# Optimization experiments

Hardware: AMD Instinct MI355X
Metric: run time of the kernel (lower is better)

The kernel has to match this reference:

```python
import jax, jax.numpy as jnp
import numpy as np

B, S, D, H = 2, 2048, 1024, 16
DK = D // H


def setup_inputs() -> dict:
    key = jax.random.key(0)
    ks = jax.random.split(key, 12)
    sc = 1.0 / np.sqrt(D)
    return {
        "q": jax.random.normal(ks[0], (B, S, D), jnp.float32),
        "k": jax.random.normal(ks[1], (B, S, D), jnp.float32),
        "v": jax.random.normal(ks[2], (B, S, D), jnp.float32),
        "mask": jax.random.randint(ks[3], (B, S), 0, 2, jnp.int32),
        "Wq": jax.random.normal(ks[4], (D, D), jnp.float32) * sc,
        "bq": jnp.zeros((D,), jnp.float32),
        "Wk": jax.random.normal(ks[5], (D, D), jnp.float32) * sc,
        "bk": jnp.zeros((D,), jnp.float32),
        "Wv": jax.random.normal(ks[6], (D, D), jnp.float32) * sc,
        "bv": jnp.zeros((D,), jnp.float32),
        "Wo": jax.random.normal(ks[7], (D, D), jnp.float32) * sc,
        "bo": jnp.zeros((D,), jnp.float32),
    }


def reference(q, k, v, mask, Wq, bq, Wk, bk, Wv, bv, Wo, bo):
    # Projections (flax nn.Dense: x @ W + b)
    query = q @ Wq + bq          # [B,S,D]
    key_ = k @ Wk + bk
    value = v @ Wv + bv
    # split heads -> [B,H,S,DK]
    def split(x):
        return x.reshape(B, S, H, DK).transpose(0, 2, 1, 3)
    qh, kh, vh = split(query), split(key_), split(value)
    scores = jnp.einsum('bhqd,bhkd->bhqk', qh, kh) / jnp.sqrt(jnp.float32(DK))
    # Faithful to source: mask=(mask==0); where(mask==0, -1e10, scores)
    # i.e. positions where ORIGINAL mask != 0 are set to -1e10.
    m = (mask == 0)[:, None, None, :]          # [B,1,1,S] bool
    scores = jnp.where(~m, jnp.float32(-1e10), scores)
    attn = jax.nn.softmax(scores, axis=-1)     # dropout deterministic (eval)
    x = jnp.einsum('bhqk,bhkd->bhqd', attn, vh)
    x = x.transpose(0, 2, 1, 3).reshape(B, S, D)
    return x @ Wo + bo
```

## Files before the change

### kernel.cpp

```cpp
#include <hip/hip_runtime.h>
#include <hip/hip_bf16.h>

typedef unsigned short u16;
typedef unsigned int u32;
typedef __attribute__((ext_vector_type(8))) __bf16 bf16x8;
typedef __attribute__((ext_vector_type(4))) float f32x4;
typedef __attribute__((ext_vector_type(16))) float f32x16;

constexpr int Bz = 2, Sq = 2048, Dm = 1024, Hn = 16, DK = 64;

__device__ __forceinline__ u16 f2bf(float f) {
    u32 u = __builtin_bit_cast(u32, f);
    return (u16)((u + 0x7FFFu + ((u >> 16) & 1u)) >> 16);
}

__device__ __forceinline__ u32 pack_bf16(float a, float b) {
#if __has_builtin(__builtin_amdgcn_cvt_pk_bf16_f32)
    return __builtin_bit_cast(u32, __builtin_amdgcn_cvt_pk_bf16_f32(a, b));
#else
    return (u32)f2bf(a) | ((u32)f2bf(b) << 16);
#endif
}

__device__ __forceinline__ bf16x8 lds_frag(const u16* p) {
    return __builtin_bit_cast(bf16x8, *(const uint4*)p);
}
__device__ __forceinline__ bf16x8 gfrag(const u16* p) {
    return __builtin_bit_cast(bf16x8, *(const uint4*)p);
}
__device__ __forceinline__ int swz(int r) { return (r ^ (r >> 3)) & 7; }

__device__ __forceinline__ void gll16(const u16* g, u16* l) {
    __builtin_amdgcn_global_load_lds(
        (const __attribute__((address_space(1))) void*)g,
        (__attribute__((address_space(3))) void*)l, 16, 0, 0);
}

__global__ __launch_bounds__(256) void mha_prep(
    const float* __restrict__ q, const float* __restrict__ k,
    const float* __restrict__ v,
    const float* __restrict__ w0, const float* __restrict__ w1,
    const float* __restrict__ w2, const float* __restrict__ w3,
    const int* __restrict__ mask,
    u16* __restrict__ qkv_dst, u16* __restrict__ wt_dst,
    float* __restrict__ biasg, int* __restrict__ compg, int* __restrict__ nkg)
{
    __shared__ float tl[64 * 65];
    __shared__ int sc[256];
    const int z = blockIdx.z, tid = threadIdx.x;
    if (z < 3) {
        const float* s = (z == 0) ? q : (z == 1) ? k : v;
        u16* d = qkv_dst + (size_t)z * 4 * 1024 * 1024;
        size_t i = ((size_t)blockIdx.x * 256 + tid) * 8;
        float4 a = *(const float4*)(s + i);
        float4 b = *(const float4*)(s + i + 4);
        *(uint4*)(d + i) = make_uint4(pack_bf16(a.x, a.y), pack_bf16(a.z, a.w),
                                      pack_bf16(b.x, b.y), pack_bf16(b.z, b.w));
        return;
    }
    const int bx = blockIdx.x;
    if (bx >= 1026) return;
    if (bx >= 1024) {
        const int b = bx - 1024;
        const int* mp = mask + b * Sq;
        int4 m0_ = ((const int4*)mp)[tid * 2];
        int4 m1_ = ((const int4*)mp)[tid * 2 + 1];
        int a[8];
        a[0] = (m0_.x == 0); a[1] = (m0_.y == 0); a[2] = (m0_.z == 0); a[3] = (m0_.w == 0);
        a[4] = (m1_.x == 0); a[5] = (m1_.y == 0); a[6] = (m1_.z == 0); a[7] = (m1_.w == 0);
        int cnt = 0;
#pragma unroll
        for (int j = 0; j < 8; j++) cnt += a[j];
        sc[tid] = cnt;
        __syncthreads();
        for (int off = 1; off < 256; off <<= 1) {
            int u = (tid >= off) ? sc[tid - off] : 0;
            int vv = sc[tid];
            __syncthreads();
            sc[tid] = vv + u;
            __syncthreads();
        }
        const int incl = sc[tid];
        const int nk = sc[255];
        int pa = incl - cnt;
        int pi = nk + tid * 8 - pa;
        int* cp = compg + b * Sq;
        float* bbp = biasg + b * Sq;
#pragma unroll
        for (int j = 0; j < 8; j++) {
            int pos = a[j] ? pa++ : pi++;
            cp[tid * 8 + j] = pos;
            bbp[pos] = a[j] ? 0.f : -1.44269504e10f;
        }
        if (tid == 0) nkg[b] = nk;
        return;
    }
    const int zi = bx >> 8, t = bx & 255, tr = t >> 4, tc = t & 15;
    const float* src = (zi == 0) ? w0 : (zi == 1) ? w1 : (zi == 2) ? w2 : w3;
    u16* d = wt_dst + (size_t)zi * Dm * Dm;
    {
        int r = tid >> 2, cq = (tid & 3) * 16;
        const float* sp = src + (size_t)(tr * 64 + r) * Dm + tc * 64 + cq;
#pragma unroll
        for (int j = 0; j < 4; j++) {
            float4 vv = *(const float4*)(sp + j * 4);
            tl[r * 65 + cq + j * 4 + 0] = vv.x;
            tl[r * 65 + cq + j * 4 + 1] = vv.y;
            tl[r * 65 + cq + j * 4 + 2] = vv.z;
            tl[r * 65 + cq + j * 4 + 3] = vv.w;
        }
    }
    __syncthreads();
    {
        int rr = tid >> 2, cc = (tid & 3) * 16;
        u16* dp = d + (size_t)(tc * 64 + rr) * Dm + tr * 64 + cc;
        u32 px[8];
#pragma unroll
        for (int j = 0; j < 8; j++)
            px[j] = pack_bf16(tl[(cc + 2 * j) * 65 + rr], tl[(cc + 2 * j + 1) * 65 + rr]);
        *(uint4*)dp       = make_uint4(px[0], px[1], px[2], px[3]);
        *(uint4*)(dp + 8) = make_uint4(px[4], px[5], px[6], px[7]);
    }
}

__device__ __forceinline__ void gemm_core_128128(
    const u16* __restrict__ Ab, const u16* __restrict__ Bb,
    u16* As, u16* Bs, f32x4 (&acc)[4][4])
{
    const int tid = threadIdx.x, lane = tid & 63;
    const int wm = (tid >> 7) & 1, wn = (tid >> 6) & 1;
    const int frow = lane & 15, quad = lane >> 4;

#pragma unroll
    for (int mi = 0; mi < 4; mi++)
#pragma unroll
        for (int ni = 0; ni < 4; ni++) acc[mi][ni] = (f32x4){0.f, 0.f, 0.f, 0.f};

    for (int k0 = 0; k0 < 1024; k0 += 64) {
#pragma unroll
        for (int i = 0; i < 4; i++) {
            int id = tid + i * 256, r = id >> 3, c = id & 7;
            gll16(Ab + (size_t)r * 1024 + k0 + (c ^ swz(r)) * 8, As + (size_t)id * 8);
        }
#pragma unroll
        for (int i = 0; i < 4; i++) {
            int id = tid + i * 256, r = id >> 3, c = id & 7;
            gll16(Bb + (size_t)r * 1024 + k0 + (c ^ swz(r)) * 8, Bs + (size_t)id * 8);
        }
        __syncthreads();
#pragma unroll
        for (int ks = 0; ks < 2; ks++) {
            bf16x8 af[4], bfr[4];
#pragma unroll
            for (int mi = 0; mi < 4; mi++) {
                int r = wm * 64 + mi * 16 + frow;
                af[mi] = lds_frag(As + r * 64 + ((ks * 4 + quad) ^ swz(r)) * 8);
            }
#pragma unroll
            for (int ni = 0; ni < 4; ni++) {
                int r = wn * 64 + ni * 16 + frow;
                bfr[ni] = lds_frag(Bs + r * 64 + ((ks * 4 + quad) ^ swz(r)) * 8);
            }
#pragma unroll
            for (int mi = 0; mi < 4; mi++)
#pragma unroll
                for (int ni = 0; ni < 4; ni++)
                    acc[mi][ni] = __builtin_amdgcn_mfma_f32_16x16x32_bf16(
                        af[mi], bfr[ni], acc[mi][ni], 0, 0, 0);
        }
        __syncthreads();
    }
}

__device__ __forceinline__ void gemm_core_12864(
    const u16* __restrict__ Ab, const u16* __restrict__ Bb,
    u16* As, u16* Bs, f32x4 (&acc)[4][2])
{
    const int tid = threadIdx.x, lane = tid & 63;
    const int wm = (tid >> 7) & 1, wn = (tid >> 6) & 1;
    const int frow = lane & 15, quad = lane >> 4;

#pragma unroll
    for (int mi = 0; mi < 4; mi++)
#pragma unroll
        for (int ni = 0; ni < 2; ni++) acc[mi][ni] = (f32x4){0.f, 0.f, 0.f, 0.f};

    for (int k0 = 0; k0 < 1024; k0 += 64) {
#pragma unroll
        for (int i = 0; i < 4; i++) {
            int id = tid + i * 256, r = id >> 3, c = id & 7;
            gll16(Ab + (size_t)r * 1024 + k0 + (c ^ swz(r)) * 8, As + (size_t)id * 8);
        }
#pragma unroll
        for (int i = 0; i < 2; i++) {
            int id = tid + i * 256, r = id >> 3, c = id & 7;
            gll16(Bb + (size_t)r * 1024 + k0 + (c ^ swz(r)) * 8, Bs + (size_t)id * 8);
        }
        __syncthreads();
#pragma unroll
        for (int ks = 0; ks < 2; ks++) {
            bf16x8 af[4], bfr[2];
#pragma unroll
            for (int mi = 0; mi < 4; mi++) {
                int r = wm * 64 + mi * 16 + frow;
                af[mi] = lds_frag(As + r * 64 + ((ks * 4 + quad) ^ swz(r)) * 8);
            }
#pragma unroll
            for (int ni = 0; ni < 2; ni++) {
                int r = wn * 32 + ni * 16 + frow;
                bfr[ni] = lds_frag(Bs + r * 64 + ((ks * 4 + quad) ^ swz(r)) * 8);
            }
#pragma unroll
            for (int mi = 0; mi < 4; mi++)
#pragma unroll
                for (int ni = 0; ni < 2; ni++)
                    acc[mi][ni] = __builtin_amdgcn_mfma_f32_16x16x32_bf16(
                        af[mi], bfr[ni], acc[mi][ni], 0, 0, 0);
        }
        __syncthreads();
    }
}

__global__ __launch_bounds__(256, 3) void mha_proj_qkv(
    const u16* __restrict__ Qb, const u16* __restrict__ Kb, const u16* __restrict__ Vb,
    const u16* __restrict__ Wqt, const u16* __restrict__ Wkt, const u16* __restrict__ Wvt,
    const float* __restrict__ bq, const float* __restrict__ bk, const float* __restrict__ bv,
    const int* __restrict__ comp,
    u16* __restrict__ Qh, u16* __restrict__ Kh, u16* __restrict__ Vt)
{
    __shared__ __align__(16) u16 As[128 * 64];
    __shared__ __align__(16) u16 Bs[128 * 64];
    const int z = blockIdx.z, bx = blockIdx.x;
    const u16* Ab; const u16* Bb; const float* bias;
    int m0, n0;
    if (z < 2) {
        m0 = (bx & 31) * 128;
        n0 = (bx >> 5) * 128;
        Ab = ((z == 0) ? Qb : Kb) + (size_t)m0 * Dm;
        Bb = ((z == 0) ? Wqt : Wkt) + (size_t)n0 * Dm;
        bias = (z == 0) ? bq : bk;
    } else {
        m0 = (bx >> 5) * 128;
        n0 = (bx & 31) * 128;
        Ab = Wvt + (size_t)m0 * Dm;
        Bb = Vb + (size_t)n0 * Dm;
        bias = bv;
    }

    f32x4 acc[4][4];
    gemm_core_128128(Ab, Bb, As, Bs, acc);

    const int tid = threadIdx.x, lane = tid & 63;
    const int wm = (tid >> 7) & 1, wn = (tid >> 6) & 1;
    const int frow = lane & 15, quad = lane >> 4;
    u16* dstq = (z == 0) ? Qh : Kh;
#pragma unroll
    for (int mi = 0; mi < 4; mi++)
#pragma unroll
        for (int ni = 0; ni < 4; ni++)
#pragma unroll
            for (int r = 0; r < 4; r++) {
                int i = m0 + wm * 64 + mi * 16 + quad * 4 + r;
                int j = n0 + wn * 64 + ni * 16 + frow;
                if (z < 2) {
                    float val = acc[mi][ni][r] + bias[j];
                    int b = i >> 11, s = i & (Sq - 1);
                    int h = j >> 6, dk = j & (DK - 1);
                    int srow = (z == 1) ? comp[b * Sq + s] : s;
                    dstq[((size_t)(b * Hn + h) * Sq + srow) * DK + dk] = f2bf(val);
                } else {
                    float val = acc[mi][ni][r] + bias[i];
                    int h = i >> 6, dk = i & (DK - 1);
                    int bj = j >> 11, s = j & (Sq - 1);
                    int cs = comp[bj * Sq + s];
                    int sp = (cs & ~12) | ((cs & 4) << 1) | ((cs & 8) >> 1);
                    Vt[((size_t)(bj * Hn + h) * DK + dk) * Sq + sp] = f2bf(val);
                }
            }
}

__global__ __launch_bounds__(512, 4) void mha_attn(
    const u16* __restrict__ Qh, const u16* __restrict__ Kh, const u16* __restrict__ Vt,
    const int* __restrict__ nkg, u16* __restrict__ X)
{
    const int bh = blockIdx.x;
    const int b = bh >> 4;
    const int q0 = blockIdx.y * 64;
    const int tid = threadIdx.x, lane = tid & 63, w = tid >> 6;
    const int wq = w & 1, p = w >> 1;
    const int qc = lane & 31, half = lane >> 5;
    constexpr float C2 = 0.125f * 1.44269504f;

    __shared__ __align__(16) u16 SB[2 * 16384];
    __shared__ float lsl[256];

    const u16* Qp = Qh + (size_t)bh * Sq * DK;
    const u16* Kp = Kh + (size_t)bh * Sq * DK;
    const u16* Vp = Vt + (size_t)bh * DK * Sq;
    const int nk = nkg[b];
    const int nt = (nk + 127) >> 7;

    bf16x8 qf[4];
    {
        const u16* qrow = Qp + (size_t)(q0 + wq * 32 + qc) * DK + half * 8;
#pragma unroll
        for (int kc = 0; kc < 4; kc++) qf[kc] = gfrag(qrow + kc * 16);
    }

    const int idA = tid, idB = tid + 512;
    const u16* ksA = Kp + (size_t)(idA >> 3) * DK + ((idA & 7) ^ swz(idA >> 3)) * 8;
    const u16* ksB = Kp + (size_t)(idB >> 3) * DK + ((idB & 7) ^ swz(idB >> 3)) * 8;
    const u16* vsA = Vp + (size_t)(idA >> 4) * Sq + (((idA & 15) ^ ((idA >> 4) & 15)) * 8);
    const u16* vsB = Vp + (size_t)(idB >> 4) * Sq + (((idB & 15) ^ ((idB >> 4) & 15)) * 8);
    u16* kdA = SB + idA * 8;
    u16* kdB = SB + idB * 8;
    u16* vdA = SB + 8192 + idA * 8;
    u16* vdB = SB + 8192 + idB * 8;

    auto stage = [&](int cur, int kb) {
        const int co = cur * 16384;
        gll16(ksA + (size_t)kb * DK, kdA + co);
        gll16(ksB + (size_t)kb * DK, kdB + co);
        gll16(vsA + kb, vdA + co);
        gll16(vsB + kb, vdB + co);
    };

    const int kr = p * 32 + qc;
    int kfo[4];
#pragma unroll
    for (int kc = 0; kc < 4; kc++)
        kfo[kc] = kr * 64 + (((kc * 2 + half) ^ swz(kr)) * 8);
    int vfo0[2], vfo1[2];
#pragma unroll
    for (int kc = 0; kc < 2; kc++) {
        int ch = p * 4 + kc * 2 + half;
        vfo0[kc] = qc * 128 + ((ch ^ (qc & 15)) * 8);
        vfo1[kc] = (32 + qc) * 128 + ((ch ^ (qc & 15)) * 8);
    }
    const int kbias = p * 32 + 4 * half;

    float l_l = 0.f;
    f32x16 o0, o1;
#pragma unroll
    for (int i = 0; i < 16; i++) { o0[i] = 0.f; o1[i] = 0.f; }

    stage(0, 0);
    for (int it = 0; it < nt; it++) {
        const int cur = it & 1;
        if (it + 1 < nt) {
            stage(cur ^ 1, (it + 1) * 128);
            asm volatile("s_waitcnt vmcnt(4)" ::: "memory");
        } else {
            asm volatile("s_waitcnt vmcnt(0)" ::: "memory");
        }
        __builtin_amdgcn_sched_barrier(0);
        __builtin_amdgcn_s_barrier();

        const u16* Kl = SB + cur * 16384;
        const u16* Vl = Kl + 8192;

        f32x16 sT;
#pragma unroll
        for (int i = 0; i < 16; i++) sT[i] = 0.f;
        __builtin_amdgcn_s_setprio(1);
#pragma unroll
        for (int kc = 0; kc < 4; kc++) {
            bf16x8 ka = lds_frag(Kl + kfo[kc]);
            sT = __builtin_amdgcn_mfma_f32_32x32x16_bf16(ka, qf[kc], sT, 0, 0, 0);
        }
        __builtin_amdgcn_s_setprio(0);

        const int thr = nk - it * 128 - kbias;
        float t[16], rs = 0.f;
#pragma unroll
        for (int g = 0; g < 4; g++) {
#pragma unroll
            for (int r = 0; r < 4; r++) {
                float bb = (8 * g + r < thr) ? 0.f : -1.44269504e10f;
                float a = __builtin_amdgcn_exp2f(fmaf(sT[g * 4 + r], C2, bb));
                t[g * 4 + r] = a; rs += a;
            }
        }
        l_l += rs;

        u32 pk[8];
#pragma unroll
        for (int i = 0; i < 8; i++) pk[i] = pack_bf16(t[2 * i], t[2 * i + 1]);

        __builtin_amdgcn_s_setprio(1);
#pragma unroll
        for (int kc = 0; kc < 2; kc++) {
            bf16x8 pf = __builtin_bit_cast(bf16x8,
                make_uint4(pk[4 * kc], pk[4 * kc + 1], pk[4 * kc + 2], pk[4 * kc + 3]));
            bf16x8 va0 = lds_frag(Vl + vfo0[kc]);
            bf16x8 va1 = lds_frag(Vl + vfo1[kc]);
            o0 = __builtin_amdgcn_mfma_f32_32x32x16_bf16(va0, pf, o0, 0, 0, 0);
            o1 = __builtin_amdgcn_mfma_f32_32x32x16_bf16(va1, pf, o1, 0, 0, 0);
        }
        __builtin_amdgcn_s_setprio(0);
        __builtin_amdgcn_s_barrier();
    }

    l_l += __shfl_xor(l_l, 32);
    float* fcb = (float*)SB;
    if (p >= 2) {
        float* fc = fcb + (size_t)(wq * 2 + (p & 1)) * 2048;
#pragma unroll
        for (int r = 0; r < 16; r++) fc[r * 64 + lane] = o0[r];
#pragma unroll
        for (int r = 0; r < 16; r++) fc[(16 + r) * 64 + lane] = o1[r];
        lsl[(wq * 2 + (p & 1)) * 64 + lane] = l_l;
    }
    __syncthreads();
    if (p < 2) {
        float* fc = fcb + (size_t)(wq * 2 + p) * 2048;
#pragma unroll
        for (int r = 0; r < 16; r++) o0[r] += fc[r * 64 + lane];
#pragma unroll
        for (int r = 0; r < 16; r++) o1[r] += fc[(16 + r) * 64 + lane];
        l_l += lsl[(wq * 2 + p) * 64 + lane];
    }
    if (p == 1) {
        float* fc = fcb + (size_t)(wq * 2 + 1) * 2048;
#pragma unroll
        for (int r = 0; r < 16; r++) fc[r * 64 + lane] = o0[r];
#pragma unroll
        for (int r = 0; r < 16; r++) fc[(16 + r) * 64 + lane] = o1[r];
        lsl[(wq * 2 + 1) * 64 + lane] = l_l;
    }
    __syncthreads();
    if (p == 0) {
        float* fc = fcb + (size_t)(wq * 2 + 1) * 2048;
#pragma unroll
        for (int r = 0; r < 16; r++) o0[r] += fc[r * 64 + lane];
#pragma unroll
        for (int r = 0; r < 16; r++) o1[r] += fc[(16 + r) * 64 + lane];
        l_l += lsl[(wq * 2 + 1) * 64 + lane];
        float inv = 1.0f / l_l;
        const int qg = q0 + wq * 32 + qc;
        u16* Xp = X + (size_t)(b * Sq + qg) * Dm + (bh & 15) * DK;
#pragma unroll
        for (int g = 0; g < 4; g++) {
            *(uint2*)&Xp[8 * g + 4 * half] =
                make_uint2(pack_bf16(o0[g * 4 + 0] * inv, o0[g * 4 + 1] * inv),
                           pack_bf16(o0[g * 4 + 2] * inv, o0[g * 4 + 3] * inv));
            *(uint2*)&Xp[32 + 8 * g + 4 * half] =
                make_uint2(pack_bf16(o1[g * 4 + 0] * inv, o1[g * 4 + 1] * inv),
                           pack_bf16(o1[g * 4 + 2] * inv, o1[g * 4 + 3] * inv));
        }
    }
}

__global__ __launch_bounds__(256) void mha_oproj(
    const u16* __restrict__ X, const u16* __restrict__ Wot,
    const float* __restrict__ bo, float* __restrict__ out)
{
    __shared__ __align__(16) u16 As[128 * 64];
    __shared__ __align__(16) u16 Bs[64 * 64];
    const int bx = blockIdx.x;
    const int m0 = (bx & 31) * 128, n0 = (bx >> 5) * 64;
    f32x4 acc[4][2];
    gemm_core_12864(X + (size_t)m0 * Dm, Wot + (size_t)n0 * Dm, As, Bs, acc);
    const int tid = threadIdx.x, lane = tid & 63;
    const int wm = (tid >> 7) & 1, wn = (tid >> 6) & 1;
    const int frow = lane & 15, quad = lane >> 4;
#pragma unroll
    for (int mi = 0; mi < 4; mi++)
#pragma unroll
        for (int ni = 0; ni < 2; ni++)
#pragma unroll
            for (int r = 0; r < 4; r++) {
                int m = m0 + wm * 64 + mi * 16 + quad * 4 + r;
                int n = n0 + wn * 32 + ni * 16 + frow;
                out[(size_t)m * Dm + n] = acc[mi][ni][r] + bo[n];
            }
}

extern "C" void kernel_launch(void* const* d_in, const int* in_sizes, int n_in,
                              void* d_out, int out_size, void* d_ws, size_t ws_size,
                              hipStream_t stream)
{
    const float* qin  = (const float*)d_in[0];
    const float* kin  = (const float*)d_in[1];
    const float* vin  = (const float*)d_in[2];
    const int*   mask = (const int*)d_in[3];
    const float* Wq   = (const float*)d_in[4];
    const float* bq   = (const float*)d_in[5];
    const float* Wk   = (const float*)d_in[6];
    const float* bk   = (const float*)d_in[7];
    const float* Wv   = (const float*)d_in[8];
    const float* bv   = (const float*)d_in[9];
    const float* Wo   = (const float*)d_in[10];
    const float* bo   = (const float*)d_in[11];
    float* out = (float*)d_out;

    u16* ws = (u16*)d_ws;
    const size_t MW = (size_t)Dm * Dm;
    const size_t MT = (size_t)Bz * Sq * Dm;
    u16* Wqt = ws;
    u16* Wkt = ws + MW;
    u16* Wvt = ws + 2 * MW;
    u16* Wot = ws + 3 * MW;
    u16* Qb  = ws + 4 * MW;
    u16* Kb  = Qb + MT;
    u16* Vb  = Kb + MT;
    u16* Qh  = Vb + MT;
    u16* Kh  = Qh + MT;
    u16* Vt  = Kh + MT;
    float* biasg = (float*)(Vt + MT);
    int*   compg = (int*)(biasg + Bz * Sq);
    int*   nkg   = (int*)(compg + Bz * Sq);
    u16* X   = Qb;

    hipLaunchKernelGGL(mha_prep, dim3(2048, 1, 4), dim3(256), 0, stream,
                       qin, kin, vin, Wq, Wk, Wv, Wo, mask, Qb, Wqt, biasg, compg, nkg);
    hipLaunchKernelGGL(mha_proj_qkv, dim3(256, 1, 3), dim3(256), 0, stream,
                       Qb, Kb, Vb, Wqt, Wkt, Wvt, bq, bk, bv, compg, Qh, Kh, Vt);
    hipLaunchKernelGGL(mha_attn, dim3(32, 32), dim3(512), 0, stream,
                       Qh, Kh, Vt, nkg, X);
    hipLaunchKernelGGL(mha_oproj, dim3(512), dim3(256), 0, stream,
                       X, Wot, bo, out);
}
```

Measured before the change: 217.5 us.

## Gather compacted K/V rows in projection and skip fully masked tiles

The prep kernel now builds an inverse compaction map (compacted position to source row) instead of a forward map and bias. The QKV projection gathers K and V input rows through this map, so the output is written already compacted. Tiles lying entirely beyond the padded count of unmasked keys return early, skipping the K and V projection work for masked positions. The cost is indirect row addressing in the global-to-LDS loads. Rows past the valid count but inside the last padded tile are still computed from masked positions, and the attention kernel must tolerate unwritten rows beyond that padding.

```diff
diff --git a/kernel.cpp b/kernel.cpp
--- a/kernel.cpp
+++ b/kernel.cpp
@@ -43,7 +43,7 @@
     const float* __restrict__ w2, const float* __restrict__ w3,
     const int* __restrict__ mask,
     u16* __restrict__ qkv_dst, u16* __restrict__ wt_dst,
-    float* __restrict__ biasg, int* __restrict__ compg, int* __restrict__ nkg)
+    int* __restrict__ invcg, int* __restrict__ nkg)
 {
     __shared__ float tl[64 * 65];
     __shared__ int sc[256];
@@ -84,13 +84,11 @@
         const int nk = sc[255];
         int pa = incl - cnt;
         int pi = nk + tid * 8 - pa;
-        int* cp = compg + b * Sq;
-        float* bbp = biasg + b * Sq;
+        int* icp = invcg + b * Sq;
 #pragma unroll
         for (int j = 0; j < 8; j++) {
             int pos = a[j] ? pa++ : pi++;
-            cp[tid * 8 + j] = pos;
-            bbp[pos] = a[j] ? 0.f : -1.44269504e10f;
+            icp[pos] = tid * 8 + j;
         }
         if (tid == 0) nkg[b] = nk;
         return;
@@ -125,6 +123,7 @@
 
 __device__ __forceinline__ void gemm_core_128128(
     const u16* __restrict__ Ab, const u16* __restrict__ Bb,
+    const int (&arow)[4], const int (&brow)[4],
     u16* As, u16* Bs, f32x4 (&acc)[4][4])
 {
     const int tid = threadIdx.x, lane = tid & 63;
@@ -140,12 +139,12 @@
 #pragma unroll
         for (int i = 0; i < 4; i++) {
             int id = tid + i * 256, r = id >> 3, c = id & 7;
-            gll16(Ab + (size_t)r * 1024 + k0 + (c ^ swz(r)) * 8, As + (size_t)id * 8);
+            gll16(Ab + (size_t)arow[i] * 1024 + k0 + (c ^ swz(r)) * 8, As + (size_t)id * 8);
         }
 #pragma unroll
         for (int i = 0; i < 4; i++) {
             int id = tid + i * 256, r = id >> 3, c = id & 7;
-            gll16(Bb + (size_t)r * 1024 + k0 + (c ^ swz(r)) * 8, Bs + (size_t)id * 8);
+            gll16(Bb + (size_t)brow[i] * 1024 + k0 + (c ^ swz(r)) * 8, Bs + (size_t)id * 8);
         }
         __syncthreads();
 #pragma unroll
@@ -225,32 +224,62 @@
     const u16* __restrict__ Qb, const u16* __restrict__ Kb, const u16* __restrict__ Vb,
     const u16* __restrict__ Wqt, const u16* __restrict__ Wkt, const u16* __restrict__ Wvt,
     const float* __restrict__ bq, const float* __restrict__ bk, const float* __restrict__ bv,
-    const int* __restrict__ comp,
+    const int* __restrict__ invc, const int* __restrict__ nkg,
     u16* __restrict__ Qh, u16* __restrict__ Kh, u16* __restrict__ Vt)
 {
     __shared__ __align__(16) u16 As[128 * 64];
     __shared__ __align__(16) u16 Bs[128 * 64];
     const int z = blockIdx.z, bx = blockIdx.x;
+    const int tid = threadIdx.x;
     const u16* Ab; const u16* Bb; const float* bias;
     int m0, n0;
     if (z < 2) {
         m0 = (bx & 31) * 128;
         n0 = (bx >> 5) * 128;
-        Ab = ((z == 0) ? Qb : Kb) + (size_t)m0 * Dm;
-        Bb = ((z == 0) ? Wqt : Wkt) + (size_t)n0 * Dm;
+        Ab = (z == 0) ? Qb : Kb;
+        Bb = (z == 0) ? Wqt : Wkt;
         bias = (z == 0) ? bq : bk;
     } else {
         m0 = (bx >> 5) * 128;
         n0 = (bx & 31) * 128;
-        Ab = Wvt + (size_t)m0 * Dm;
-        Bb = Vb + (size_t)n0 * Dm;
+        Ab = Wvt;
+        Bb = Vb;
         bias = bv;
     }
 
+    int arow[4], brow[4];
+#pragma unroll
+    for (int i = 0; i < 4; i++) {
+        int r = (tid + i * 256) >> 3;
+        arow[i] = m0 + r;
+        brow[i] = n0 + r;
+    }
+    if (z == 1) {
+        const int bb = m0 >> 11, pos0 = m0 & 2047;
+        const int nkp = (nkg[bb] + 127) & ~127;
+        if (pos0 >= nkp) return;
+        const int* ic = invc + ((size_t)bb << 11) + pos0;
+#pragma unroll
+        for (int i = 0; i < 4; i++) {
+            int r = (tid + i * 256) >> 3;
+            arow[i] = (bb << 11) + ic[r];
+        }
+    } else if (z == 2) {
+        const int bj = n0 >> 11, pos0 = n0 & 2047;
+        const int nkp = (nkg[bj] + 127) & ~127;
+        if (pos0 >= nkp) return;
+        const int* ic = invc + ((size_t)bj << 11) + pos0;
+#pragma unroll
+        for (int i = 0; i < 4; i++) {
+            int r = (tid + i * 256) >> 3;
+            brow[i] = (bj << 11) + ic[r];
+        }
+    }
+
     f32x4 acc[4][4];
-    gemm_core_128128(Ab, Bb, As, Bs, acc);
-
-    const int tid = threadIdx.x, lane = tid & 63;
+    gemm_core_128128(Ab, Bb, arow, brow, As, Bs, acc);
+
+    const int lane = tid & 63;
     const int wm = (tid >> 7) & 1, wn = (tid >> 6) & 1;
     const int frow = lane & 15, quad = lane >> 4;
     u16* dstq = (z == 0) ? Qh : Kh;
@@ -266,13 +295,11 @@
                     float val = acc[mi][ni][r] + bias[j];
                     int b = i >> 11, s = i & (Sq - 1);
                     int h = j >> 6, dk = j & (DK - 1);
-                    int srow = (z == 1) ? comp[b * Sq + s] : s;
-                    dstq[((size_t)(b * Hn + h) * Sq + srow) * DK + dk] = f2bf(val);
+                    dstq[((size_t)(b * Hn + h) * Sq + s) * DK + dk] = f2bf(val);
                 } else {
                     float val = acc[mi][ni][r] + bias[i];
                     int h = i >> 6, dk = i & (DK - 1);
-                    int bj = j >> 11, s = j & (Sq - 1);
-                    int cs = comp[bj * Sq + s];
+                    int bj = j >> 11, cs = j & (Sq - 1);
                     int sp = (cs & ~12) | ((cs & 4) << 1) | ((cs & 8) >> 1);
                     Vt[((size_t)(bj * Hn + h) * DK + dk) * Sq + sp] = f2bf(val);
                 }
@@ -507,15 +534,14 @@
     u16* Qh  = Vb + MT;
     u16* Kh  = Qh + MT;
     u16* Vt  = Kh + MT;
-    float* biasg = (float*)(Vt + MT);
-    int*   compg = (int*)(biasg + Bz * Sq);
-    int*   nkg   = (int*)(compg + Bz * Sq);
+    int*   invcg = (int*)(Vt + MT);
+    int*   nkg   = invcg + Bz * Sq;
     u16* X   = Qb;
 
     hipLaunchKernelGGL(mha_prep, dim3(2048, 1, 4), dim3(256), 0, stream,
-                       qin, kin, vin, Wq, Wk, Wv, Wo, mask, Qb, Wqt, biasg, compg, nkg);
+                       qin, kin, vin, Wq, Wk, Wv, Wo, mask, Qb, Wqt, invcg, nkg);
     hipLaunchKernelGGL(mha_proj_qkv, dim3(256, 1, 3), dim3(256), 0, stream,
-                       Qb, Kb, Vb, Wqt, Wkt, Wvt, bq, bk, bv, compg, Qh, Kh, Vt);
+                       Qb, Kb, Vb, Wqt, Wkt, Wvt, bq, bk, bv, invcg, nkg, Qh, Kh, Vt);
     hipLaunchKernelGGL(mha_attn, dim3(32, 32), dim3(512), 0, stream,
                        Qh, Kh, Vt, nkg, X);
     hipLaunchKernelGGL(mha_oproj, dim3(512), dim3(256), 0, stream,
```

Measured after the change: 211.0 us. 1.03x faster.
